# Optimization experiments

Hardware: AMD Instinct MI355X
Metric: run time of the kernel (lower is better)

Reference implementation:

```python
import jax, jax.numpy as jnp
import numpy as np

B, S, P, D = 128, 64, 32, 256   # batch, seq_len, pad_size, input_size
E, H, L, A, O = 256, 128, 2, 1, 2  # embed, hidden, n_layers, att_dim, output
INITRANGE = 0.1


def setup_inputs() -> dict:
    key = jax.random.key(0)
    ks = jax.random.split(key, 12)
    u = lambda k, shape: jax.random.uniform(k, shape, jnp.float32, -INITRANGE, INITRANGE)
    return {
        "inputs": jax.random.normal(ks[0], (B, S, P, D), jnp.float32),
        "conv_w": u(ks[1], (D,)),          # Conv1d(1,1,kernel=D) weight (output length is 1)
        "conv_b": u(ks[2], (1,)),
        "embed_w": u(ks[3], (E, D)),       # Linear(D,E,bias=False)
        "gru_Wih": u(ks[4], (L, 2, 3 * H, E)),  # [layer, direction, 3H, in] (E == 2H)
        "gru_Whh": u(ks[5], (L, 2, 3 * H, H)),
        "gru_bih": u(ks[6], (L, 2, 3 * H)),
        "gru_bhh": u(ks[7], (L, 2, 3 * H)),
        "att_w1": u(ks[8], (A, 2 * H)),    # Linear(2H, att_dim, bias=False)
        "lin_w": u(ks[9], (O, 2 * H)),
        "lin_b": u(ks[10], (O,)),
        "batch_size": B,
    }


def _gru_layer(x, Wih, Whh, bih, bhh, reverse):
    # x: [B,S,Din]; torch GRU cell semantics.
    xg = jnp.einsum('bsd,gd->sbg', x, Wih) + bih  # precompute input gates [S,B,3H]
    h0 = jnp.zeros((x.shape[0], Whh.shape[1]), x.dtype)

    def step(h, xg_t):
        gh = h @ Whh.T + bhh
        xr, xz, xn = jnp.split(xg_t, 3, axis=-1)
        hr, hz, hn = jnp.split(gh, 3, axis=-1)
        r = jax.nn.sigmoid(xr + hr)
        z = jax.nn.sigmoid(xz + hz)
        n = jnp.tanh(xn + r * hn)
        h_new = (1.0 - z) * n + z * h
        return h_new, h_new

    _, hs = jax.lax.scan(step, h0, xg, reverse=reverse)  # [S,B,H], time-aligned
    return jnp.swapaxes(hs, 0, 1)  # [B,S,H]


def _forward(inputs, conv_w, conv_b, embed_w, gru_Wih, gru_Whh, gru_bih, gru_bhh,
             att_w1, lin_w, lin_b, batch_size):
    # convolutional_layer: conv output length is 1 -> per-event scalar dot product,
    # then bmm gives a weighted sum of events within each visit.
    s = jnp.einsum('bspk,k->bsp', inputs, conv_w) + conv_b[0]      # [B,S,P]
    conv_all = jnp.einsum('bsp,bspk->bsk', s, inputs)               # [B,S,D]
    # embedding_layer: Linear(D,E) + Hardtanh
    x = jnp.clip(conv_all @ embed_w.T, -1.0, 1.0)                   # [B,S,E]
    # bidirectional multi-layer GRU, h0 = zeros (dropout_p = 0 -> identity)
    for l in range(L):
        f = _gru_layer(x, gru_Wih[l, 0], gru_Whh[l, 0], gru_bih[l, 0], gru_bhh[l, 0], False)
        b = _gru_layer(x, gru_Wih[l, 1], gru_Whh[l, 1], gru_bih[l, 1], gru_bhh[l, 1], True)
        x = jnp.concatenate([f, b], axis=-1)                        # [B,S,2H]
    states = x
    # add_attention: per-step Linear(2H, att_dim) + softmax over att_dim (nn.Softmax on [B,A])
    alpha = jax.nn.softmax(jnp.einsum('bsh,ah->bsa', states, att_w1), axis=-1)
    alpha = jnp.swapaxes(alpha, 1, 2)                               # [B,A,S]
    context = jnp.einsum('bas,bsh->bah', alpha, states).reshape(batch_size, -1)  # [B, A*2H]
    out = jax.nn.softmax(context @ lin_w.T + lin_b, axis=-1)        # [B,O]
    return out, states, context, alpha


def reference(inputs, conv_w, conv_b, embed_w, gru_Wih, gru_Whh, gru_bih, gru_bhh,
              att_w1, lin_w, lin_b, batch_size):
    return _forward(inputs, conv_w, conv_b, embed_w, gru_Wih, gru_Whh, gru_bih,
                    gru_bhh, att_w1, lin_w, lin_b, batch_size)
```

## Files before the change

kernel.cpp:

```cpp
#include <hip/hip_runtime.h>


using u16 = unsigned short;
using u32 = unsigned int;

typedef __bf16    bf16x8 __attribute__((ext_vector_type(8)));
typedef _Float16  f16x8  __attribute__((ext_vector_type(8)));
typedef float     f32x4  __attribute__((ext_vector_type(4)));

__device__ __forceinline__ float bf2f(u16 u) {
  union { u32 i; float f; } v; v.i = ((u32)u) << 16; return v.f;
}
__device__ __forceinline__ u16 f2bf(float f) {
  union { float f; u32 i; } v; v.f = f;
  u32 i = v.i;
  u32 r = (i + 0x7FFFu + ((i >> 16) & 1u)) >> 16;
  return (u16)r;
}
__device__ __forceinline__ float sigm(float x) { return 1.f / (1.f + __expf(-x)); }
__device__ __forceinline__ float tanh_f(float x) { return 1.f - 2.f / (1.f + __expf(2.f * x)); }

__global__ __launch_bounds__(256) void k_conv(
    const float* __restrict__ inp, const float* __restrict__ cw,
    const float* __restrict__ cb, u16* __restrict__ chi, u16* __restrict__ clo,
    const float* __restrict__ embw, const float* __restrict__ Wih,
    u16* __restrict__ embHi, u16* __restrict__ embLo, u16* __restrict__ wihB) {
  __shared__ float tile[32 * 256];
  __shared__ float cwf[256];
  __shared__ float s_p[32];
  const int bs  = blockIdx.x;
  const int tid = threadIdx.x;
  const float* src = inp + (size_t)bs * 8192;
#pragma unroll
  for (int i = 0; i < 8; i++) {
    int idx = i * 1024 + tid * 4;
    *(float4*)&tile[idx] = *(const float4*)&src[idx];
  }
  cwf[tid] = cw[tid];
  if (bs < 1536) {
    const int i = bs * 256 + tid;
    if (i < 65536) {
      float v = embw[i];
      u16 h = f2bf(v);
      embHi[i] = h;
      embLo[i] = f2bf(v - bf2f(h));
    }
    wihB[i] = f2bf(Wih[i]);
  }
  __syncthreads();
  const int wv = tid >> 6, ln = tid & 63;
  const float cbf = cb[0];
  for (int pp = 0; pp < 8; pp++) {
    int p = wv * 8 + pp;
    float part = 0.f;
#pragma unroll
    for (int q = 0; q < 4; q++) {
      int k = ln + q * 64;
      part += tile[p * 256 + k] * cwf[k];
    }
    for (int off = 32; off; off >>= 1) part += __shfl_xor(part, off, 64);
    if (ln == 0) s_p[p] = part + cbf;
  }
  __syncthreads();
  float acc = 0.f;
  const int k = tid;
#pragma unroll
  for (int p = 0; p < 32; p++) acc += s_p[p] * tile[p * 256 + k];
  u16 hi = f2bf(acc);
  float lo = acc - bf2f(hi);
  chi[(size_t)bs * 256 + k] = hi;
  clo[(size_t)bs * 256 + k] = f2bf(lo);
}

template <bool HAS_ALO, bool HAS_WLO, bool HAS_BIAS, bool CLIP, bool OUT_BF16>
__global__ __launch_bounds__(256) void k_gemm(
    const u16* __restrict__ A, const u16* __restrict__ Alo,
    const u16* __restrict__ W, const u16* __restrict__ Wlo,
    const float* __restrict__ bias,
    void* __restrict__ Cout, int M, int N, int K) {
  const int LDT = 56;
  __shared__ u16 As[64 * 56];
  __shared__ u16 La[64 * 56];
  __shared__ u16 Ws[64 * 56];
  __shared__ u16 Lw[64 * 56];
  const int tid = threadIdx.x;
  const int m0 = blockIdx.x * 64, n0 = blockIdx.y * 64;
  const int wv = tid >> 6, ln = tid & 63;
  const int lm = ln & 15, lk = (ln >> 4) * 8;
  const int srow = tid >> 2, sgrp = tid & 3;

  const size_t aRow = (size_t)(m0 + srow) * K + sgrp * 8;
  const size_t wRow = (size_t)(n0 + srow) * K + sgrp * 8;

  f32x4 acc[4];
#pragma unroll
  for (int nt = 0; nt < 4; nt++) acc[nt] = (f32x4){0.f, 0.f, 0.f, 0.f};

  uint4 rA = *(const uint4*)&A[aRow];
  uint4 rW = *(const uint4*)&W[wRow];
  uint4 rLa, rLw;
  if (HAS_ALO) rLa = *(const uint4*)&Alo[aRow];
  if (HAS_WLO) rLw = *(const uint4*)&Wlo[wRow];

  const int nIter = K >> 5;
  for (int it = 0; it < nIter; it++) {
    __syncthreads();
    *(uint4*)&As[srow * LDT + sgrp * 8] = rA;
    *(uint4*)&Ws[srow * LDT + sgrp * 8] = rW;
    if (HAS_ALO) *(uint4*)&La[srow * LDT + sgrp * 8] = rLa;
    if (HAS_WLO) *(uint4*)&Lw[srow * LDT + sgrp * 8] = rLw;
    if (it + 1 < nIter) {
      const int kc = (it + 1) * 32;
      rA = *(const uint4*)&A[aRow + kc];
      rW = *(const uint4*)&W[wRow + kc];
      if (HAS_ALO) rLa = *(const uint4*)&Alo[aRow + kc];
      if (HAS_WLO) rLw = *(const uint4*)&Wlo[wRow + kc];
    }
    __syncthreads();

    bf16x8 af = *(const bf16x8*)&As[(wv * 16 + lm) * LDT + lk];
    bf16x8 bfr[4];
#pragma unroll
    for (int nt = 0; nt < 4; nt++)
      bfr[nt] = *(const bf16x8*)&Ws[(nt * 16 + lm) * LDT + lk];
#pragma unroll
    for (int nt = 0; nt < 4; nt++)
      acc[nt] = __builtin_amdgcn_mfma_f32_16x16x32_bf16(af, bfr[nt], acc[nt], 0, 0, 0);
    if (HAS_ALO) {
      bf16x8 lf = *(const bf16x8*)&La[(wv * 16 + lm) * LDT + lk];
#pragma unroll
      for (int nt = 0; nt < 4; nt++)
        acc[nt] = __builtin_amdgcn_mfma_f32_16x16x32_bf16(lf, bfr[nt], acc[nt], 0, 0, 0);
    }
    if (HAS_WLO) {
#pragma unroll
      for (int nt = 0; nt < 4; nt++) {
        bf16x8 wl = *(const bf16x8*)&Lw[(nt * 16 + lm) * LDT + lk];
        acc[nt] = __builtin_amdgcn_mfma_f32_16x16x32_bf16(af, wl, acc[nt], 0, 0, 0);
      }
    }
  }

  const int rbase = m0 + wv * 16 + (ln >> 4) * 4;
#pragma unroll
  for (int nt = 0; nt < 4; nt++) {
    const int col = n0 + nt * 16 + lm;
    const float bv = HAS_BIAS ? bias[col] : 0.f;
#pragma unroll
    for (int r = 0; r < 4; r++) {
      float v = acc[nt][r] + bv;
      if (CLIP) v = fminf(fmaxf(v, -1.f), 1.f);
      const int row = rbase + r;
      if (OUT_BF16)
        ((u16*)Cout)[(size_t)row * N + col] = f2bf(v);
      else
        ((float*)Cout)[(size_t)row * N + col] = v;
    }
  }
}

__global__ __launch_bounds__(512, 2) void k_gru(
    const float* __restrict__ xg,
    const float* __restrict__ WhhL,
    const float* __restrict__ bhhL,
    u16* __restrict__ st_bf,
    float* __restrict__ st_f,
    float* __restrict__ ctx) {
  __shared__ __attribute__((aligned(16))) _Float16 hbHi[2][128];
  __shared__ __attribute__((aligned(16))) _Float16 hbLo[2][128];

  const int b   = blockIdx.x >> 1;
  const int dir = blockIdx.x & 1;
  const int tid = threadIdx.x;
  const int w   = tid >> 6, l = tid & 63;
  const int lm  = l & 15;
  const int kw  = (l >> 4) * 8;
  const int d   = w * 16 + lm;

  f16x8 whi[3][4], wlo[3][4];
#pragma unroll
  for (int tt = 0; tt < 3; tt++) {
#pragma unroll
    for (int kt = 0; kt < 4; kt++) {
      const int row = (tt * 8 + w) * 16 + lm;
      const float* p = WhhL + ((size_t)(dir * 384 + row)) * 128 + kt * 32 + kw;
      union { f16x8 v; _Float16 s[8]; } Wh, Wl;
#pragma unroll
      for (int j = 0; j < 8; j++) {
        float v = p[j];
        _Float16 h = (_Float16)v;
        Wh.s[j] = h;
        Wl.s[j] = (_Float16)(v - (float)h);
      }
      whi[tt][kt] = Wh.v;
      wlo[tt][kt] = Wl.v;
    }
  }
  float bhr = 0.f, bhz = 0.f, bhn = 0.f;
  if (l < 16) {
    bhr = bhhL[dir * 384 + d];
    bhz = bhhL[dir * 384 + 128 + d];
    bhn = bhhL[dir * 384 + 256 + d];
  }
  if (tid < 128) { hbHi[0][tid] = (_Float16)0.f; hbLo[0][tid] = (_Float16)0.f; }

  const float* xbase = xg + (size_t)(b * 64) * 768 + dir * 384 + d;
  float xr = 0.f, xz = 0.f, xn = 0.f;
  if (l < 16) {
    const int t0 = dir ? 63 : 0;
    xr = xbase[t0 * 768];
    xz = xbase[t0 * 768 + 128];
    xn = xbase[t0 * 768 + 256];
  }
  float hold = 0.f, csum = 0.f;
  __syncthreads();

  int cur = 0;
  for (int ti = 0; ti < 64; ti++) {
    const int t = dir ? (63 - ti) : ti;
    float nxr = 0.f, nxz = 0.f, nxn = 0.f;
    if (l < 16 && ti < 63) {
      const int tn = dir ? (62 - ti) : (ti + 1);
      nxr = xbase[tn * 768];
      nxz = xbase[tn * 768 + 128];
      nxn = xbase[tn * 768 + 256];
    }
    const _Float16* hsrc = (l & 1) ? hbLo[cur] : hbHi[cur];
    f16x8 af[4];
#pragma unroll
    for (int kt = 0; kt < 4; kt++)
      af[kt] = *(const f16x8*)&hsrc[kt * 32 + kw];

    f32x4 aH[3], aL[3];
#pragma unroll
    for (int tt = 0; tt < 3; tt++) {
      aH[tt] = (f32x4){0.f, 0.f, 0.f, 0.f};
      aL[tt] = (f32x4){0.f, 0.f, 0.f, 0.f};
    }
#pragma unroll
    for (int kt = 0; kt < 4; kt++) {
#pragma unroll
      for (int tt = 0; tt < 3; tt++) {
        aH[tt] = __builtin_amdgcn_mfma_f32_16x16x32_f16(af[kt], whi[tt][kt], aH[tt], 0, 0, 0);
        aL[tt] = __builtin_amdgcn_mfma_f32_16x16x32_f16(af[kt], wlo[tt][kt], aL[tt], 0, 0, 0);
      }
    }
    const int nxt = cur ^ 1;
    if (l < 16) {
      const float ghr = aH[0][0] + aH[0][1] + aL[0][0] + aL[0][1];
      const float ghz = aH[1][0] + aH[1][1] + aL[1][0] + aL[1][1];
      const float ghn = aH[2][0] + aH[2][1] + aL[2][0] + aL[2][1];
      const float rg = sigm(xr + bhr + ghr);
      const float zg = sigm(xz + bhz + ghz);
      const float ng = tanh_f(xn + rg * (ghn + bhn));
      const float hn = (1.f - zg) * ng + zg * hold;
      hold = hn;
      csum += hn;
      const _Float16 hh = (_Float16)hn;
      hbHi[nxt][d] = hh;
      hbLo[nxt][d] = (_Float16)(hn - (float)hh);
      const size_t oi = (size_t)(b * 64 + t) * 256 + dir * 128 + d;
      if (st_bf) st_bf[oi] = f2bf(hn);
      if (st_f)  st_f[oi]  = hn;
    }
    asm volatile("s_waitcnt lgkmcnt(0)" ::: "memory");
    __builtin_amdgcn_s_barrier();
    cur = nxt;
    xr = nxr; xz = nxz; xn = nxn;
  }
  if (ctx != nullptr && l < 16)
    ctx[(size_t)b * 256 + dir * 128 + d] = csum;
}

__global__ __launch_bounds__(64) void k_final(
    const float* __restrict__ ctx, const float* __restrict__ lw,
    const float* __restrict__ lb, float* __restrict__ out,
    float* __restrict__ alpha) {
  const int b = blockIdx.x;
  const int l = threadIdx.x;
  float a0 = 0.f, a1 = 0.f;
#pragma unroll
  for (int q = 0; q < 4; q++) {
    const int k = q * 64 + l;
    const float c = ctx[b * 256 + k];
    a0 += c * lw[k];
    a1 += c * lw[256 + k];
  }
  for (int off = 32; off; off >>= 1) {
    a0 += __shfl_xor(a0, off, 64);
    a1 += __shfl_xor(a1, off, 64);
  }
  alpha[b * 64 + l] = 1.0f;
  if (l == 0) {
    a0 += lb[0];
    a1 += lb[1];
    const float m = fmaxf(a0, a1);
    const float e0 = __expf(a0 - m), e1 = __expf(a1 - m);
    const float s = e0 + e1;
    out[2 * b]     = e0 / s;
    out[2 * b + 1] = e1 / s;
  }
}

extern "C" void kernel_launch(void* const* d_in, const int* in_sizes, int n_in,
                              void* d_out, int out_size, void* d_ws, size_t ws_size,
                              hipStream_t stream) {
  const float* inp   = (const float*)d_in[0];
  const float* convw = (const float*)d_in[1];
  const float* convb = (const float*)d_in[2];
  const float* embw  = (const float*)d_in[3];
  const float* Wih   = (const float*)d_in[4];
  const float* Whh   = (const float*)d_in[5];
  const float* bih   = (const float*)d_in[6];
  const float* bhh   = (const float*)d_in[7];
  const float* lw    = (const float*)d_in[9];
  const float* lb    = (const float*)d_in[10];

  char* ws = (char*)d_ws;
  u16*   convHi = (u16*)(ws);
  u16*   convLo = (u16*)(ws + 4194304u);
  u16*   xbuf   = (u16*)(ws + 8388608u);
  u16*   embHi  = (u16*)(ws + 12582912u);
  u16*   embLo  = (u16*)(ws + 12713984u);
  u16*   wihB   = (u16*)(ws + 12845056u);
  float* xgbuf  = (float*)(ws + 13631488u);
  u16*   states0 = convHi;

  float* outp    = (float*)d_out;
  float* statesO = outp + 256;
  float* ctxO    = outp + 2097408;
  float* alphaO  = outp + 2130176;

  k_conv<<<8192, 256, 0, stream>>>(inp, convw, convb, convHi, convLo,
                                   embw, Wih, embHi, embLo, wihB);

  dim3 gE(128, 4);
  k_gemm<true, true, false, true, true><<<gE, 256, 0, stream>>>(
      convHi, convLo, embHi, embLo, nullptr, xbuf, 8192, 256, 256);

  dim3 gX(128, 12);
  k_gemm<false, false, true, false, false><<<gX, 256, 0, stream>>>(
      xbuf, nullptr, wihB, nullptr, bih, xgbuf, 8192, 768, 256);

  k_gru<<<256, 512, 0, stream>>>(xgbuf, Whh, bhh, states0, nullptr, nullptr);

  k_gemm<false, false, true, false, false><<<gX, 256, 0, stream>>>(
      states0, nullptr, wihB + 196608, nullptr, bih + 768, xgbuf, 8192, 768, 256);

  k_gru<<<256, 512, 0, stream>>>(xgbuf, Whh + 98304, bhh + 768,
                                 nullptr, statesO, ctxO);

  k_final<<<128, 64, 0, stream>>>(ctxO, lw, lb, outp, alphaO);
}
```

Before: 528.2 us.

## Fuse GRU input-gate projection GEMM into the recurrent GRU kernel

Removes the separate input-projection GEMM launches before each GRU layer. Each GRU block now loads its sequence's 64x256 bf16 input into LDS, computes its direction's 64x384 input-gate matrix with bf16 MFMAs, and writes it to a private global scratch slice before starting the recurrence. This saves two kernel launches and the full xg write/read round trip through a separate kernel. In exchange, the projection runs on only 256 blocks, each block reloads W_ih, and it adds a large LDS buffer that may lower occupancy.

```diff
diff --git a/kernel.cpp b/kernel.cpp
--- a/kernel.cpp
+++ b/kernel.cpp
@@ -160,12 +160,16 @@
 }
 
 __global__ __launch_bounds__(512, 2) void k_gru(
-    const float* __restrict__ xg,
+    const u16* __restrict__ xsrc,
+    const u16* __restrict__ wihL,
+    const float* __restrict__ bihL,
     const float* __restrict__ WhhL,
     const float* __restrict__ bhhL,
+    float* __restrict__ xg,
     u16* __restrict__ st_bf,
     float* __restrict__ st_f,
     float* __restrict__ ctx) {
+  __shared__ __attribute__((aligned(16))) u16 xt[64 * 264];
   __shared__ __attribute__((aligned(16))) _Float16 hbHi[2][128];
   __shared__ __attribute__((aligned(16))) _Float16 hbLo[2][128];
 
@@ -196,6 +200,43 @@
       wlo[tt][kt] = Wl.v;
     }
   }
+
+  const u16*   wihD = wihL + (size_t)dir * 98304;
+  const float* bihD = bihL + dir * 384;
+  float*       xgc  = xg + (size_t)(b * 2 + dir) * 24576;
+  {
+    const u16* xrow = xsrc + (size_t)(b * 64) * 256;
+#pragma unroll
+    for (int it = 0; it < 4; it++) {
+      const int idx = it * 512 + tid;
+      const int r = idx >> 5, c8 = (idx & 31) * 8;
+      *(uint4*)&xt[r * 264 + c8] = *(const uint4*)&xrow[r * 256 + c8];
+    }
+    __syncthreads();
+#pragma unroll
+    for (int tt = 0; tt < 3; tt++) {
+      const int nt = tt * 8 + w;
+      bf16x8 bfr[8];
+#pragma unroll
+      for (int kk = 0; kk < 8; kk++)
+        bfr[kk] = *(const bf16x8*)&wihD[(size_t)(nt * 16 + lm) * 256 + kk * 32 + kw];
+      const float bv = bihD[nt * 16 + lm];
+      const int col = nt * 16 + lm;
+#pragma unroll
+      for (int mt = 0; mt < 4; mt++) {
+        f32x4 a4 = (f32x4){0.f, 0.f, 0.f, 0.f};
+#pragma unroll
+        for (int kk = 0; kk < 8; kk++) {
+          bf16x8 af = *(const bf16x8*)&xt[(mt * 16 + lm) * 264 + kk * 32 + kw];
+          a4 = __builtin_amdgcn_mfma_f32_16x16x32_bf16(af, bfr[kk], a4, 0, 0, 0);
+        }
+        const int trow = mt * 16 + (l >> 4) * 4;
+#pragma unroll
+        for (int r = 0; r < 4; r++)
+          xgc[(size_t)(trow + r) * 384 + col] = a4[r] + bv;
+      }
+    }
+  }
   float bhr = 0.f, bhz = 0.f, bhn = 0.f;
   if (l < 16) {
     bhr = bhhL[dir * 384 + d];
@@ -203,17 +244,17 @@
     bhn = bhhL[dir * 384 + 256 + d];
   }
   if (tid < 128) { hbHi[0][tid] = (_Float16)0.f; hbLo[0][tid] = (_Float16)0.f; }
-
-  const float* xbase = xg + (size_t)(b * 64) * 768 + dir * 384 + d;
+  __syncthreads();
+
+  const float* xbase = xgc + d;
   float xr = 0.f, xz = 0.f, xn = 0.f;
   if (l < 16) {
     const int t0 = dir ? 63 : 0;
-    xr = xbase[t0 * 768];
-    xz = xbase[t0 * 768 + 128];
-    xn = xbase[t0 * 768 + 256];
+    xr = xbase[t0 * 384];
+    xz = xbase[t0 * 384 + 128];
+    xn = xbase[t0 * 384 + 256];
   }
   float hold = 0.f, csum = 0.f;
-  __syncthreads();
 
   int cur = 0;
   for (int ti = 0; ti < 64; ti++) {
@@ -221,9 +262,9 @@
     float nxr = 0.f, nxz = 0.f, nxn = 0.f;
     if (l < 16 && ti < 63) {
       const int tn = dir ? (62 - ti) : (ti + 1);
-      nxr = xbase[tn * 768];
-      nxz = xbase[tn * 768 + 128];
-      nxn = xbase[tn * 768 + 256];
+      nxr = xbase[tn * 384];
+      nxz = xbase[tn * 384 + 128];
+      nxn = xbase[tn * 384 + 256];
     }
     const _Float16* hsrc = (l & 1) ? hbLo[cur] : hbHi[cur];
     f16x8 af[4];
@@ -338,16 +379,11 @@
   k_gemm<true, true, false, true, true><<<gE, 256, 0, stream>>>(
       convHi, convLo, embHi, embLo, nullptr, xbuf, 8192, 256, 256);
 
-  dim3 gX(128, 12);
-  k_gemm<false, false, true, false, false><<<gX, 256, 0, stream>>>(
-      xbuf, nullptr, wihB, nullptr, bih, xgbuf, 8192, 768, 256);
-
-  k_gru<<<256, 512, 0, stream>>>(xgbuf, Whh, bhh, states0, nullptr, nullptr);
-
-  k_gemm<false, false, true, false, false><<<gX, 256, 0, stream>>>(
-      states0, nullptr, wihB + 196608, nullptr, bih + 768, xgbuf, 8192, 768, 256);
-
-  k_gru<<<256, 512, 0, stream>>>(xgbuf, Whh + 98304, bhh + 768,
+  k_gru<<<256, 512, 0, stream>>>(xbuf, wihB, bih, Whh, bhh, xgbuf,
+                                 states0, nullptr, nullptr);
+
+  k_gru<<<256, 512, 0, stream>>>(states0, wihB + 196608, bih + 768,
+                                 Whh + 98304, bhh + 768, xgbuf,
                                  nullptr, statesO, ctxO);
 
   k_final<<<128, 64, 0, stream>>>(ctxO, lw, lb, outp, alphaO);
```

New measurement: 528.1 us (median of 2 runs). About the same (-0.0%).
